# Performance work log

Measured on AMD Instinct MI355X. Metric: run time of the kernel, lower is better.

Reference implementation:

```python
import jax, jax.numpy as jnp
import numpy as np
import math

B, IN, D, H, DEPTH, E, K = 16384, 128, 512, 8, 3, 8, 2
FF, EH = 4 * D, 256          # ffn width = 4*d_model; expert hidden fixed at 256 in source
EPSILON = 0.1                # forward() default epsilon (exploration mixing)
LN_EPS = 1e-5


def _ln(x, w, b):
    m = x.mean(-1, keepdims=True)
    v = x.var(-1, keepdims=True)  # biased variance, matching nn.LayerNorm
    return (x - m) / jnp.sqrt(v + LN_EPS) * w + b


def setup_inputs() -> dict:
    key = jax.random.key(0)
    ks = jax.random.split(key, 16)
    s = 0.02
    rn = lambda k, shape: jax.random.normal(k, shape, jnp.float32) * s
    return dict(
        x=jax.random.normal(ks[0], (B, IN), jnp.float32),
        embed_w=rn(ks[1], (IN, D)), embed_b=jnp.zeros((D,), jnp.float32),
        ln1_w=jnp.ones((DEPTH, D), jnp.float32), ln1_b=jnp.zeros((DEPTH, D), jnp.float32),
        inproj_w=rn(ks[2], (DEPTH, 3 * D, D)), inproj_b=jnp.zeros((DEPTH, 3 * D), jnp.float32),
        outproj_w=rn(ks[3], (DEPTH, D, D)), outproj_b=jnp.zeros((DEPTH, D), jnp.float32),
        ln2_w=jnp.ones((DEPTH, D), jnp.float32), ln2_b=jnp.zeros((DEPTH, D), jnp.float32),
        ffn_w1=rn(ks[4], (DEPTH, D, FF)), ffn_b1=jnp.zeros((DEPTH, FF), jnp.float32),
        ffn_w2=rn(ks[5], (DEPTH, FF, D)), ffn_b2=jnp.zeros((DEPTH, D), jnp.float32),
        router_w=rn(ks[6], (D, E)), router_b=jnp.zeros((E,), jnp.float32),
        exp_w1=rn(ks[7], (E, D, EH)), exp_b1=jnp.zeros((E, EH), jnp.float32),
        exp_w2=rn(ks[8], (E, EH, D)), exp_b2=jnp.zeros((E, D), jnp.float32),
        head_ln_w=jnp.ones((D,), jnp.float32), head_ln_b=jnp.zeros((D,), jnp.float32),
        head_w=rn(ks[9], (D, 1)), head_b=jnp.zeros((1,), jnp.float32),
    )


def reference(x, embed_w, embed_b, ln1_w, ln1_b, inproj_w, inproj_b,
              outproj_w, outproj_b, ln2_w, ln2_b, ffn_w1, ffn_b1, ffn_w2, ffn_b2,
              router_w, router_b, exp_w1, exp_b1, exp_w2, exp_b2,
              head_ln_w, head_ln_b, head_w, head_b):
    h = x @ embed_w + embed_b                       # [B, D]; unsqueeze(1) -> seq_len == 1
    for l in range(DEPTH):
        g = _ln(h, ln1_w[l], ln1_b[l])
        qkv = g @ inproj_w[l].T + inproj_b[l]       # [B, 3D]
        # seq_len == 1: softmax over the single key is exactly 1, so attn(h,h,h) == out_proj(V)
        v = qkv[:, 2 * D:]
        a = v @ outproj_w[l].T + outproj_b[l]
        h = h + a
        g = _ln(h, ln2_w[l], ln2_b[l])
        h = h + jax.nn.gelu(g @ ffn_w1[l] + ffn_b1[l], approximate=False) @ ffn_w2[l] + ffn_b2[l]
    z = h                                           # squeeze(1)

    # WaggleGate
    logits = z @ router_w + router_b                # [B, E]
    probs = jax.nn.softmax(logits, axis=-1)
    probs = (1.0 - EPSILON) * probs + EPSILON / E
    wts, idx = jax.lax.top_k(probs, K)              # [B, K]
    load = probs.mean(0)
    aux = (load * jnp.log(load * E + 1e-9)).sum() / math.log(E + 1e-9)

    # dense all-expert compute + sparse top-k combine (same math as per-sample dispatch)
    hmid = jax.nn.gelu(jnp.einsum('bd,edh->ebh', z, exp_w1) + exp_b1[:, None, :], approximate=False)
    eo = jnp.einsum('ebh,ehd->ebd', hmid, exp_w2) + exp_b2[:, None, :]   # [E, B, D]
    gate = jnp.zeros((z.shape[0], E), z.dtype).at[
        jnp.arange(z.shape[0])[:, None], idx].add(wts)                    # [B, E]
    moe = jnp.einsum('be,ebd->bd', gate, eo)

    z = z + moe
    logit = (_ln(z, head_ln_w, head_ln_b) @ head_w + head_b)[:, 0]       # [B]
    return logit, aux
```

## Files before the change

kernel.cpp:

```cpp
#include <hip/hip_runtime.h>
#include <hip/hip_bf16.h>

#define B_TOK 16384
#define IN_DIM 128
#define D_DIM 512
#define DEPTH 3
#define NEXP 8
#define FF_DIM 2048
#define EH_DIM 256
#define MAXSLOT 34816
#define MAXT256 136
#define NHBLK 64

typedef __attribute__((ext_vector_type(8))) __bf16 bf16x8;
typedef __attribute__((ext_vector_type(4))) float f32x4;
typedef __attribute__((ext_vector_type(4))) unsigned short u16x4;
typedef __attribute__((ext_vector_type(8))) unsigned short u16x8;

__device__ __forceinline__ unsigned short f2bf(float f){
    unsigned int u = __float_as_uint(f);
    u += 0x7fffu + ((u >> 16) & 1u);
    return (unsigned short)(u >> 16);
}
__device__ __forceinline__ float bf2f(unsigned short u){
    return __uint_as_float(((unsigned int)u) << 16);
}
__device__ __forceinline__ float geluf(float x){
    float x2 = x * x;
    float y  = x * (0.79788456080287f + 0.03567740814183f * x2);
    y = fminf(fmaxf(y, -15.0f), 15.0f);
    float e = __expf(2.0f * y);
    float th = 1.0f - 2.0f / (e + 1.0f);
    return 0.5f * x * (1.0f + th);
}
__device__ __forceinline__ void gload_lds16(const void* g, void* l){
    __builtin_amdgcn_global_load_lds((const __attribute__((address_space(1))) unsigned int*)g,
                                     (__attribute__((address_space(3))) unsigned int*)l,
                                     16, 0, 0);
}
__device__ __forceinline__ int xcd_swizzle(int orig, int nwg){
    const int q = nwg >> 3, r = nwg & 7;
    const int xcd = orig & 7;
    const int idx = orig >> 3;
    return (xcd < r ? xcd*(q+1) : r*(q+1) + (xcd-r)*q) + idx;
}

__global__ void zero_kernel(int* a, int na, int* b, int nb){
    const int i = blockIdx.x * blockDim.x + threadIdx.x;
    if (i < na) a[i] = 0;
    if (i < nb) b[i] = 0;
}

struct ConvSeg { const float* src; unsigned short* dst; int n4; };
struct ConvArgs { ConvSeg seg[2]; };

__global__ void convert_kernel(ConvArgs a){
    const int stride = gridDim.x * blockDim.x;
    const int tid = blockIdx.x * blockDim.x + threadIdx.x;
    for (int s = 0; s < 2; ++s){
        const f32x4* src = (const f32x4*)a.seg[s].src;
        u16x4* dst = (u16x4*)a.seg[s].dst;
        const int n4 = a.seg[s].n4;
        for (int i = tid; i < n4; i += stride){
            f32x4 v = src[i];
            u16x4 o;
            o[0] = f2bf(v[0]); o[1] = f2bf(v[1]); o[2] = f2bf(v[2]); o[3] = f2bf(v[3]);
            dst[i] = o;
        }
    }
}

struct TSeg { const float* src; unsigned short* dst; int K; int N; int tileStart; };
struct TArgs { TSeg seg[26]; };

__global__ void transpose_kernel(TArgs a){
    __shared__ float t[32][33];
    const int tile = blockIdx.x;
    int s = 0;
    #pragma unroll 1
    while (s < 25 && tile >= a.seg[s+1].tileStart) ++s;
    const TSeg sg = a.seg[s];
    const int local = tile - sg.tileStart;
    const int tilesN = sg.N >> 5;
    const int k0 = (local / tilesN) << 5;
    const int n0 = (local % tilesN) << 5;
    const int tx = threadIdx.x & 31;
    const int ty = threadIdx.x >> 5;
    #pragma unroll
    for (int j = 0; j < 4; ++j)
        t[ty + j*8][tx] = sg.src[(size_t)(k0 + ty + j*8) * sg.N + n0 + tx];
    __syncthreads();
    #pragma unroll
    for (int j = 0; j < 4; ++j){
        const int n = ty + j*8;
        sg.dst[(size_t)(n0 + n) * sg.K + k0 + tx] = f2bf(t[tx][n]);
    }
}

__global__ void foldb_kernel(const float* __restrict__ outproj_w, const float* __restrict__ outproj_b,
                             const float* __restrict__ inproj_b, float* __restrict__ bfold){
    const int l = blockIdx.x, n = threadIdx.x;
    const float* Wo = outproj_w + ((size_t)l*D_DIM + n)*D_DIM;
    const float* bv = inproj_b + l*3*D_DIM + 2*D_DIM;
    float acc = outproj_b[l*D_DIM + n];
    for (int j = 0; j < D_DIM; ++j) acc += Wo[j]*bv[j];
    bfold[l*D_DIM + n] = acc;
}

__global__ void __launch_bounds__(256, 2)
gemm_bt(const unsigned short* __restrict__ A, const unsigned short* __restrict__ Bt,
        const float* __restrict__ bias, unsigned short* __restrict__ out, int NB, int N, int K)
{
    __shared__ unsigned short sh[32768];
    const int nwg = gridDim.x;
    const int wg  = xcd_swizzle(blockIdx.x, nwg);
    const int bn  = wg % NB;
    const int bm  = wg / NB;

    const int tid  = threadIdx.x;
    const int lane = tid & 63;
    const int wave = tid >> 6;
    const int wm = (wave >> 1) << 6;
    const int wn = (wave & 1) << 6;

    f32x4 acc[4][4] = {};

    const unsigned short* Abase = A + (size_t)bm * 128 * K;
    const unsigned short* Bbase = Bt + (size_t)bn * 128 * K;
    const int soff = tid * 16;

    auto STAGE = [&](int b, int kt){
        char* Ab = (char*)(sh + b*16384);
        char* Bb = (char*)(sh + b*16384 + 8192);
        #pragma unroll
        for (int s = 0; s < 4; ++s){
            const int off = s*4096 + soff;
            const int row = off >> 7, colb = off & 127;
            gload_lds16((const char*)(Abase + (size_t)row*K + kt) + colb, Ab + off);
        }
        #pragma unroll
        for (int s = 0; s < 4; ++s){
            const int off = s*4096 + soff;
            const int row = off >> 7, colb = off & 127;
            gload_lds16((const char*)(Bbase + (size_t)row*K + kt) + colb, Bb + off);
        }
    };
    auto COMPUTE = [&](int b){
        const unsigned short* Ab = sh + b*16384;
        const unsigned short* Bb = sh + b*16384 + 8192;
        #pragma unroll
        for (int ks = 0; ks < 2; ++ks){
            const int k0 = ks*32 + ((lane>>4)<<3);
            bf16x8 af[4], bfr[4];
            #pragma unroll
            for (int i=0;i<4;i++) af[i]  = *(const bf16x8*)&Ab[(wm + i*16 + (lane&15))*64 + k0];
            #pragma unroll
            for (int j=0;j<4;j++) bfr[j] = *(const bf16x8*)&Bb[(wn + j*16 + (lane&15))*64 + k0];
            #pragma unroll
            for (int i=0;i<4;i++)
                #pragma unroll
                for (int j=0;j<4;j++)
                    acc[i][j] = __builtin_amdgcn_mfma_f32_16x16x32_bf16(af[i], bfr[j], acc[i][j], 0, 0, 0);
        }
    };

    STAGE(0, 0);
    __syncthreads();
    const int nk = K >> 6;
    int cur = 0;
    for (int i = 0; i < nk; ++i){
        if (i + 1 < nk) STAGE(cur ^ 1, (i + 1) << 6);
        COMPUTE(cur);
        __syncthreads();
        cur ^= 1;
    }

    const int r0 = ((lane>>4)<<2);
    const int cc = lane & 15;
    unsigned short* Ct = sh;
    float bcol[4];
    #pragma unroll
    for (int j=0;j<4;j++) bcol[j] = bias[bn*128 + wn + j*16 + cc];
    #pragma unroll
    for (int i=0;i<4;i++)
        #pragma unroll
        for (int r=0;r<4;r++){
            const int rl = wm + i*16 + r0 + r;
            #pragma unroll
            for (int j=0;j<4;j++)
                Ct[rl*128 + wn + j*16 + cc] = f2bf(acc[i][j][r] + bcol[j]);
        }
    __syncthreads();
    const int orow = tid >> 4;
    const int ocol = (tid & 15) * 8;
    #pragma unroll
    for (int p = 0; p < 8; ++p){
        const int row = p*16 + orow;
        *(u16x8*)(&out[(size_t)(bm*128 + row)*N + bn*128 + ocol]) = *(u16x8*)&Ct[row*128 + ocol];
    }
}

__global__ void __launch_bounds__(512, 2)
gemm256sq(const unsigned short* __restrict__ A, const unsigned short* __restrict__ Bt,
          const float* __restrict__ bias, unsigned short* __restrict__ out,
          int NB, int N, int K)
{
    __shared__ __align__(16) char sh[131072];
    const int nwg = gridDim.x;
    const int wg  = xcd_swizzle(blockIdx.x, nwg);
    const int bn  = wg % NB;
    const int bm  = wg / NB;
    const int m0  = bm * 256;
    const int n0  = bn * 256;

    const int tid = threadIdx.x, lane = tid & 63, wave = tid >> 6;
    const int wr = wave >> 2;
    const int wc = wave & 3;

    const int srow = wave*16 + (lane >> 3);
    const int scol = ((lane & 7) ^ (lane >> 3)) * 8;
    const unsigned short* aptr[2][2];
    const unsigned short* bptr[2][2];
    #pragma unroll
    for (int u = 0; u < 2; ++u)
        #pragma unroll
        for (int l = 0; l < 2; ++l){
            aptr[u][l] = A  + (size_t)(m0 + u*128 + srow + l*8) * K + scol;
            bptr[u][l] = Bt + (size_t)(n0 + u*128 + srow + l*8) * K + scol;
        }
    const int sdst = wave*2048 + lane*16;

    int ch[2];
    #pragma unroll
    for (int ks = 0; ks < 2; ++ks)
        ch[ks] = ((((ks<<2) + (lane>>4)) ^ (lane & 7)) << 4);
    const int arow = wr*128 + (lane & 15);
    const int brow = wc*64  + (lane & 15);

    f32x4 acc[8][4] = {};

    auto STAGE = [&](int buf, int kt){
        #pragma unroll
        for (int u = 0; u < 2; ++u)
            #pragma unroll
            for (int l = 0; l < 2; ++l)
                gload_lds16(aptr[u][l] + kt, sh + buf*32768 + u*16384 + l*1024 + sdst);
        #pragma unroll
        for (int u = 0; u < 2; ++u)
            #pragma unroll
            for (int l = 0; l < 2; ++l)
                gload_lds16(bptr[u][l] + kt, sh + 65536 + buf*32768 + u*16384 + l*1024 + sdst);
    };
    auto COMPUTE = [&](int buf){
        bf16x8 bfr[4][2];
        #pragma unroll
        for (int nf = 0; nf < 4; ++nf)
            #pragma unroll
            for (int ks = 0; ks < 2; ++ks)
                bfr[nf][ks] = *(const bf16x8*)(sh + 65536 + buf*32768 + (brow + nf*16)*128 + ch[ks]);
        #pragma unroll
        for (int mf = 0; mf < 8; ++mf){
            bf16x8 af[2];
            #pragma unroll
            for (int ks = 0; ks < 2; ++ks)
                af[ks] = *(const bf16x8*)(sh + buf*32768 + (arow + mf*16)*128 + ch[ks]);
            #pragma unroll
            for (int nf = 0; nf < 4; ++nf)
                #pragma unroll
                for (int ks = 0; ks < 2; ++ks)
                    acc[mf][nf] = __builtin_amdgcn_mfma_f32_16x16x32_bf16(af[ks], bfr[nf][ks], acc[mf][nf], 0,0,0);
        }
    };

    STAGE(0, 0);
    __syncthreads();
    const int nk = K >> 6;
    int cur = 0;
    for (int i = 0; i < nk; ++i){
        if (i + 1 < nk) STAGE(cur ^ 1, (i + 1) << 6);
        COMPUTE(cur);
        __syncthreads();
        cur ^= 1;
    }

    unsigned short* Ct = (unsigned short*)sh;
    const int r4 = (lane >> 4) * 4;
    const int cc = lane & 15;
    #pragma unroll
    for (int nf = 0; nf < 4; ++nf){
        const int col = wc*64 + nf*16 + cc;
        const float bv = bias[n0 + col];
        #pragma unroll
        for (int mf = 0; mf < 8; ++mf)
            #pragma unroll
            for (int r = 0; r < 4; ++r){
                const int row = wr*128 + mf*16 + r4 + r;
                Ct[row*256 + col] = f2bf(geluf(acc[mf][nf][r] + bv));
            }
    }
    __syncthreads();
    #pragma unroll
    for (int p = 0; p < 16; ++p){
        const int uidx = p*512 + tid;
        const int row = uidx >> 5;
        const int cu  = uidx & 31;
        *(u16x8*)(out + (size_t)(m0 + row)*N + n0 + cu*8) = *(const u16x8*)(Ct + row*256 + cu*8);
    }
}

#define G_GELU_BF16 0
#define G_BF16_RESID 1
#define G_GATED_BF16 2

template<int EPI, int MOE, int INDIRECT>
__global__ void __launch_bounds__(512, 2)
gemm256(const unsigned short* __restrict__ A, const unsigned short* __restrict__ BtG,
        const float* __restrict__ biasG, const unsigned short* __restrict__ resid,
        const int* __restrict__ tok, const int* __restrict__ offs,
        int wstride, int bstride, const float* __restrict__ gslot,
        unsigned short* __restrict__ out, int NB, int N, int K)
{
    __shared__ __align__(16) char sh[147456];
    const int nwg = gridDim.x;
    const int wg  = xcd_swizzle(blockIdx.x, nwg);
    const int bn  = wg % NB;
    const int bm  = wg / NB;
    const int m0  = bm * 256;

    const unsigned short* Bt = BtG;
    const float* bias = biasG;
    if (MOE){
        if (m0 >= offs[8]) return;
        int e = 0;
        #pragma unroll 1
        while (offs[e+1] <= m0) ++e;
        Bt   += (size_t)e * wstride;
        bias += (size_t)e * bstride;
    }

    const int tid = threadIdx.x, lane = tid & 63, wave = tid >> 6;
    const int wm = (wave >> 1) * 64;
    const int wn = (wave & 1) * 64;

    const int srow = wave*16 + (lane >> 3);
    const int scol = ((lane & 7) ^ (lane >> 3)) * 8;
    const unsigned short* aptr[2][2];
    #pragma unroll
    for (int u = 0; u < 2; ++u)
        #pragma unroll
        for (int l = 0; l < 2; ++l){
            const int r = u*128 + srow + l*8;
            const int gr = INDIRECT ? tok[m0 + r] : (m0 + r);
            aptr[u][l] = A + (size_t)gr * K + scol;
        }
    const unsigned short* bptr[2];
    #pragma unroll
    for (int l = 0; l < 2; ++l)
        bptr[l] = Bt + (size_t)(bn*128 + srow + l*8) * K + scol;
    const int sdst = wave*2048 + lane*16;

    int aoff[2], boff[2];
    #pragma unroll
    for (int ks = 0; ks < 2; ++ks){
        const int ch = (((ks<<2) + (lane>>4)) ^ (lane & 7)) << 4;
        aoff[ks] = (wm + (lane & 15))*128 + ch;
        boff[ks] = (wn + (lane & 15))*128 + ch;
    }

    f32x4 acc[4][4] = {};

    auto STAGE = [&](int buf, int kt){
        #pragma unroll
        for (int u = 0; u < 2; ++u)
            #pragma unroll
            for (int l = 0; l < 2; ++l)
                gload_lds16(aptr[u][l] + kt, sh + buf*32768 + u*16384 + l*1024 + sdst);
        #pragma unroll
        for (int l = 0; l < 2; ++l)
            gload_lds16(bptr[l] + kt, sh + 98304 + buf*16384 + l*1024 + sdst);
    };
    auto COMPUTE = [&](int buf){
        bf16x8 bfr[4][2];
        #pragma unroll
        for (int nf = 0; nf < 4; ++nf)
            #pragma unroll
            for (int ks = 0; ks < 2; ++ks)
                bfr[nf][ks] = *(const bf16x8*)(sh + 98304 + buf*16384 + nf*2048 + boff[ks]);
        #pragma unroll
        for (int mf = 0; mf < 4; ++mf){
            bf16x8 af[2];
            #pragma unroll
            for (int ks = 0; ks < 2; ++ks)
                af[ks] = *(const bf16x8*)(sh + buf*32768 + mf*2048 + aoff[ks]);
            #pragma unroll
            for (int nf = 0; nf < 4; ++nf)
                #pragma unroll
                for (int ks = 0; ks < 2; ++ks)
                    acc[mf][nf] = __builtin_amdgcn_mfma_f32_16x16x32_bf16(af[ks], bfr[nf][ks], acc[mf][nf], 0,0,0);
        }
    };

    STAGE(0, 0);
    __syncthreads();
    const int nk = K >> 6;
    int cur = 0;
    for (int i = 0; i < nk; ++i){
        if (i + 1 < nk) STAGE(cur ^ 1, (i + 1) << 6);
        COMPUTE(cur);
        __syncthreads();
        cur ^= 1;
    }

    const int r4 = (lane >> 4) * 4;
    const int cc = lane & 15;
    if (EPI == G_BF16_RESID){
        float* ctf = (float*)sh;
        #pragma unroll
        for (int nf = 0; nf < 4; ++nf){
            const float bv = bias[bn*128 + wn + nf*16 + cc];
            #pragma unroll
            for (int mf = 0; mf < 4; ++mf)
                #pragma unroll
                for (int r = 0; r < 4; ++r){
                    const int row = wm + mf*16 + r4 + r;
                    ctf[row*128 + wn + nf*16 + cc] = acc[mf][nf][r] + bv;
                }
        }
        __syncthreads();
        #pragma unroll
        for (int p = 0; p < 8; ++p){
            const int uidx = p*512 + tid;
            const int row = uidx >> 4;
            const int cu  = uidx & 15;
            const size_t gidx = (size_t)(m0 + row)*N + bn*128 + cu*8;
            u16x8 hv = *(const u16x8*)(resid + gidx);
            u16x8 o;
            #pragma unroll
            for (int j = 0; j < 8; ++j)
                o[j] = f2bf(bf2f(hv[j]) + ctf[row*128 + cu*8 + j]);
            *(u16x8*)(out + gidx) = o;
        }
    } else {
        unsigned short* ct = (unsigned short*)sh;
        #pragma unroll
        for (int nf = 0; nf < 4; ++nf){
            const float bv = bias[bn*128 + wn + nf*16 + cc];
            #pragma unroll
            for (int mf = 0; mf < 4; ++mf)
                #pragma unroll
                for (int r = 0; r < 4; ++r){
                    const int row = wm + mf*16 + r4 + r;
                    float v = acc[mf][nf][r] + bv;
                    if (EPI == G_GELU_BF16) v = geluf(v);
                    else                    v *= gslot[m0 + row];
                    ct[row*128 + wn + nf*16 + cc] = f2bf(v);
                }
        }
        __syncthreads();
        #pragma unroll
        for (int p = 0; p < 8; ++p){
            const int uidx = p*512 + tid;
            const int row = uidx >> 4;
            const int cu  = uidx & 15;
            *(u16x8*)(out + (size_t)(m0 + row)*N + bn*128 + cu*8) =
                *(const u16x8*)(ct + row*128 + cu*8);
        }
    }
}

__global__ void ln_kernel(const unsigned short* __restrict__ x, const float* __restrict__ w,
                          const float* __restrict__ b, unsigned short* __restrict__ out)
{
    const int lane = threadIdx.x & 63;
    const int wave = threadIdx.x >> 6;
    const int row  = blockIdx.x * 4 + wave;
    u16x8 hv = *(const u16x8*)(x + (size_t)row * D_DIM + lane*8);
    float v[8];
    #pragma unroll
    for (int j = 0; j < 8; ++j) v[j] = bf2f(hv[j]);
    float s = 0.f, s2 = 0.f;
    #pragma unroll
    for (int j = 0; j < 8; ++j){ s += v[j]; s2 += v[j]*v[j]; }
    #pragma unroll
    for (int o = 32; o > 0; o >>= 1){ s += __shfl_xor(s, o); s2 += __shfl_xor(s2, o); }
    const float mean = s * (1.0f/512.0f);
    const float var  = s2 * (1.0f/512.0f) - mean*mean;
    const float inv  = 1.0f / sqrtf(var + 1e-5f);
    const int k = lane*8;
    u16x8 o;
    #pragma unroll
    for (int j = 0; j < 8; ++j) o[j] = f2bf((v[j]-mean)*inv*w[k+j] + b[k+j]);
    *(u16x8*)(out + (size_t)row*D_DIM + k) = o;
}

__global__ void router_kernel(const unsigned short* __restrict__ z, const float* __restrict__ rw,
                              const float* __restrict__ rb,
                              int2* __restrict__ idx2, float2* __restrict__ wts2,
                              float* __restrict__ bsums)
{
    __shared__ float ps[4][8];
    const int lane = threadIdx.x & 63;
    const int wave = threadIdx.x >> 6;
    const int row  = blockIdx.x * 4 + wave;
    u16x8 hv = *(const u16x8*)(z + (size_t)row * D_DIM + lane*8);
    float acc[8] = {0,0,0,0,0,0,0,0};
    #pragma unroll
    for (int j = 0; j < 8; ++j){
        const float zv = bf2f(hv[j]);
        const float* wr = rw + (size_t)(lane*8 + j) * 8;
        f32x4 w0 = *(const f32x4*)wr;
        f32x4 w1 = *(const f32x4*)(wr + 4);
        acc[0] += zv*w0[0]; acc[1] += zv*w0[1]; acc[2] += zv*w0[2]; acc[3] += zv*w0[3];
        acc[4] += zv*w1[0]; acc[5] += zv*w1[1]; acc[6] += zv*w1[2]; acc[7] += zv*w1[3];
    }
    #pragma unroll
    for (int o = 32; o > 0; o >>= 1){
        #pragma unroll
        for (int e = 0; e < 8; ++e) acc[e] += __shfl_xor(acc[e], o);
    }
    if (lane == 0){
        float p[8]; float mx = -1e30f;
        #pragma unroll
        for (int e=0;e<8;e++){ p[e] = acc[e] + rb[e]; mx = fmaxf(mx, p[e]); }
        float se = 0.f;
        #pragma unroll
        for (int e=0;e<8;e++){ p[e] = expf(p[e]-mx); se += p[e]; }
        const float sc = 0.9f / se;
        #pragma unroll
        for (int e=0;e<8;e++) p[e] = p[e]*sc + 0.0125f;
        int i1 = 0;
        #pragma unroll
        for (int e=1;e<8;e++) if (p[e] > p[i1]) i1 = e;
        int i2 = (i1 == 0) ? 1 : 0;
        for (int e=i2+1;e<8;e++) if (e != i1 && p[e] > p[i2]) i2 = e;
        idx2[row] = make_int2(i1, i2);
        wts2[row] = make_float2(p[i1], p[i2]);
        #pragma unroll
        for (int e=0;e<8;e++) ps[wave][e] = p[e];
    }
    __syncthreads();
    if (threadIdx.x < 8){
        bsums[blockIdx.x*8 + threadIdx.x] =
            ps[0][threadIdx.x] + ps[1][threadIdx.x] + ps[2][threadIdx.x] + ps[3][threadIdx.x];
    }
}

__global__ void hist_kernel(const int2* __restrict__ idx2, int* __restrict__ blockHist){
    __shared__ int hc[8];
    if (threadIdx.x < 8) hc[threadIdx.x] = 0;
    __syncthreads();
    const int t = blockIdx.x * 256 + threadIdx.x;
    const int2 ii = idx2[t];
    atomicAdd(&hc[ii.x], 1);
    atomicAdd(&hc[ii.y], 1);
    __syncthreads();
    if (threadIdx.x < 8) blockHist[blockIdx.x*8 + threadIdx.x] = hc[threadIdx.x];
}

__global__ void scan_kernel(const int* __restrict__ blockHist, int* __restrict__ offs,
                            int* __restrict__ baseArr){
    if (threadIdx.x == 0){
        int counts[8];
        #pragma unroll
        for (int e=0;e<8;e++) counts[e] = 0;
        for (int b=0;b<NHBLK;b++)
            #pragma unroll
            for (int e=0;e<8;e++) counts[e] += blockHist[b*8+e];
        int o = 0; offs[0] = 0;
        int start[8];
        #pragma unroll
        for (int e=0;e<8;e++){ start[e] = o; o += (counts[e]+255)&~255; offs[e+1] = o; }
        for (int e=0;e<8;e++){
            int cur = start[e];
            for (int b=0;b<NHBLK;b++){ baseArr[b*8+e] = cur; cur += blockHist[b*8+e]; }
        }
    }
}

__global__ void assign_kernel(const int2* __restrict__ idx2, const float2* __restrict__ wts2,
                              const int* __restrict__ baseArr, int2* __restrict__ slot_map,
                              float* __restrict__ gslot, int* __restrict__ tok)
{
    __shared__ int cur[8];
    if (threadIdx.x < 8) cur[threadIdx.x] = 0;
    __syncthreads();
    const int t = blockIdx.x * 256 + threadIdx.x;
    const int2 ii = idx2[t];
    const float2 ww = wts2[t];
    const int r1 = atomicAdd(&cur[ii.x], 1);
    const int r2 = atomicAdd(&cur[ii.y], 1);
    const int s1 = baseArr[blockIdx.x*8 + ii.x] + r1;
    const int s2 = baseArr[blockIdx.x*8 + ii.y] + r2;
    slot_map[t] = make_int2(s1, s2);
    gslot[s1] = ww.x; gslot[s2] = ww.y;
    tok[s1] = t; tok[s2] = t;
}

__global__ void aux_kernel(const float* __restrict__ bsums, float* __restrict__ out_aux)
{
    __shared__ float part[256];
    const int t = threadIdx.x;
    const int e = t & 7, chunk = t >> 3;
    float s = 0.f;
    for (int blk = chunk*128; blk < chunk*128 + 128; ++blk) s += bsums[blk*8 + e];
    part[t] = s;
    __syncthreads();
    if (t < 8){
        float tot = 0.f;
        for (int c = 0; c < 32; ++c) tot += part[c*8 + t];
        part[t] = tot;
    }
    __syncthreads();
    if (t == 0){
        float aux = 0.f;
        for (int e2 = 0; e2 < 8; ++e2){
            float load = part[e2] * (1.0f/16384.0f);
            aux += load * logf(load * 8.0f + 1e-9f);
        }
        out_aux[0] = aux / 2.0794415416798357f;
    }
}

__global__ void head_kernel(const unsigned short* __restrict__ h, const unsigned short* __restrict__ eog,
                            const int2* __restrict__ slot_map,
                            const float* __restrict__ w, const float* __restrict__ b,
                            const float* __restrict__ hw, const float* __restrict__ hb,
                            float* __restrict__ out)
{
// ... 34 lines not shown
    const float* embed_b   = (const float*)d_in[2];
    const float* ln1_w     = (const float*)d_in[3];
    const float* ln1_b     = (const float*)d_in[4];
    const float* inproj_w  = (const float*)d_in[5];
    const float* inproj_b  = (const float*)d_in[6];
    const float* outproj_w = (const float*)d_in[7];
    const float* outproj_b = (const float*)d_in[8];
    const float* ln2_w     = (const float*)d_in[9];
    const float* ln2_b     = (const float*)d_in[10];
    const float* ffn_w1    = (const float*)d_in[11];
    const float* ffn_b1    = (const float*)d_in[12];
    const float* ffn_w2    = (const float*)d_in[13];
    const float* ffn_b2    = (const float*)d_in[14];
    const float* router_w  = (const float*)d_in[15];
    const float* router_b  = (const float*)d_in[16];
    const float* exp_w1    = (const float*)d_in[17];
    const float* exp_b1    = (const float*)d_in[18];
    const float* exp_w2    = (const float*)d_in[19];
    const float* exp_b2    = (const float*)d_in[20];
    const float* head_ln_w = (const float*)d_in[21];
    const float* head_ln_b = (const float*)d_in[22];
    const float* head_w    = (const float*)d_in[23];
    const float* head_b    = (const float*)d_in[24];

    char* ws = (char*)d_ws;
    unsigned short* xbf   = (unsigned short*)(ws + 0);
    unsigned short* ebf   = (unsigned short*)(ws + 4194304);
    unsigned short* wobf  = (unsigned short*)(ws + 4325376);
    unsigned short* wvtbf = (unsigned short*)(ws + 5898240);
    unsigned short* wfold = (unsigned short*)(ws + 7471104);
    unsigned short* w1t   = (unsigned short*)(ws + 9043968);
    unsigned short* w2t   = (unsigned short*)(ws + 15335424);
    unsigned short* e1t   = (unsigned short*)(ws + 21626880);
    unsigned short* e2t   = (unsigned short*)(ws + 23724032);
    unsigned short* h     = (unsigned short*)(ws + 25821184);
    unsigned short* gbf   = (unsigned short*)(ws + 42598400);
    unsigned short* ubf   = (unsigned short*)(ws + 59375616);
    unsigned short* hmidg = ubf;
    unsigned short* eog   = (unsigned short*)(ws + 77201408);
    char* MISC = ws + 126484480;
    int*    offs     = (int*)(MISC + 0);
    float*  zbias    = (float*)(MISC + 256);
    float*  bfold    = (float*)(MISC + 2304);
    int2*   idx2     = (int2*)(MISC + 8448);
    float2* wts2     = (float2*)(MISC + 139520);
    int2*   slot_map = (int2*)(MISC + 270592);
    float*  gslot    = (float*)(MISC + 401664);
    int*    tok      = (int*)(MISC + 544768);
    float*  bsums    = (float*)(MISC + 684032);
    int*    blockHist= (int*)(MISC + 815104);
    int*    baseArr  = (int*)(MISC + 817152);
    float* out = (float*)d_out;

    zero_kernel<<<(MAXSLOT + 255)/256, 256, 0, stream>>>((int*)zbias, 512, tok, MAXSLOT);

    ConvArgs ca;
    ca.seg[0] = { x, xbf, B_TOK*IN_DIM/4 };
    ca.seg[1] = { outproj_w, wobf, DEPTH*D_DIM*D_DIM/4 };
    convert_kernel<<<1024, 256, 0, stream>>>(ca);

    TArgs ta;
    int tcur = 0, ti = 0;
    ta.seg[ti] = { embed_w, ebf, IN_DIM, D_DIM, tcur };
    tcur += (IN_DIM/32)*(D_DIM/32); ++ti;
    for (int l = 0; l < DEPTH; ++l){
        ta.seg[ti] = { ffn_w1 + (size_t)l*D_DIM*FF_DIM, w1t + (size_t)l*FF_DIM*D_DIM, D_DIM, FF_DIM, tcur };
        tcur += (D_DIM/32)*(FF_DIM/32); ++ti;
    }
    for (int l = 0; l < DEPTH; ++l){
        ta.seg[ti] = { ffn_w2 + (size_t)l*FF_DIM*D_DIM, w2t + (size_t)l*D_DIM*FF_DIM, FF_DIM, D_DIM, tcur };
        tcur += (FF_DIM/32)*(D_DIM/32); ++ti;
    }
    for (int e = 0; e < NEXP; ++e){
        ta.seg[ti] = { exp_w1 + (size_t)e*D_DIM*EH_DIM, e1t + (size_t)e*EH_DIM*D_DIM, D_DIM, EH_DIM, tcur };
        tcur += (D_DIM/32)*(EH_DIM/32); ++ti;
    }
    for (int e = 0; e < NEXP; ++e){
        ta.seg[ti] = { exp_w2 + (size_t)e*EH_DIM*D_DIM, e2t + (size_t)e*D_DIM*EH_DIM, EH_DIM, D_DIM, tcur };
        tcur += (EH_DIM/32)*(D_DIM/32); ++ti;
    }
    for (int l = 0; l < DEPTH; ++l){
        ta.seg[ti] = { inproj_w + (size_t)l*3*D_DIM*D_DIM + 2*D_DIM*D_DIM,
                       wvtbf + (size_t)l*D_DIM*D_DIM, D_DIM, D_DIM, tcur };
        tcur += (D_DIM/32)*(D_DIM/32); ++ti;
    }
    transpose_kernel<<<tcur, 256, 0, stream>>>(ta);

    foldb_kernel<<<DEPTH, D_DIM, 0, stream>>>(outproj_w, outproj_b, inproj_b, bfold);

    for (int l = 0; l < DEPTH; ++l){
        gemm_bt<<<16, 256, 0, stream>>>(
            wobf + (size_t)l*D_DIM*D_DIM, wvtbf + (size_t)l*D_DIM*D_DIM,
            zbias, wfold + (size_t)l*D_DIM*D_DIM, 4, D_DIM, D_DIM);
    }

    gemm_bt<<<(D_DIM/128)*(B_TOK/128), 256, 0, stream>>>(
        xbf, ebf, embed_b, h, D_DIM/128, D_DIM, IN_DIM);

    for (int l = 0; l < DEPTH; ++l){
        ln_kernel<<<B_TOK/4, 256, 0, stream>>>(h, ln1_w + l*D_DIM, ln1_b + l*D_DIM, gbf);
        gemm256<G_BF16_RESID,0,0><<<(B_TOK/256)*(D_DIM/128), 512, 0, stream>>>(
            gbf, wfold + (size_t)l*D_DIM*D_DIM, bfold + l*D_DIM, h,
            nullptr, nullptr, 0, 0, nullptr, h, D_DIM/128, D_DIM, D_DIM);
        ln_kernel<<<B_TOK/4, 256, 0, stream>>>(h, ln2_w + l*D_DIM, ln2_b + l*D_DIM, gbf);
        gemm256sq<<<(B_TOK/256)*(FF_DIM/256), 512, 0, stream>>>(
            gbf, w1t + (size_t)l*FF_DIM*D_DIM, ffn_b1 + l*FF_DIM, ubf, FF_DIM/256, FF_DIM, D_DIM);
        gemm256<G_BF16_RESID,0,0><<<(B_TOK/256)*(D_DIM/128), 512, 0, stream>>>(
            ubf, w2t + (size_t)l*D_DIM*FF_DIM, ffn_b2 + l*D_DIM, h,
            nullptr, nullptr, 0, 0, nullptr, h, D_DIM/128, D_DIM, FF_DIM);
    }

    router_kernel<<<B_TOK/4, 256, 0, stream>>>(h, router_w, router_b, idx2, wts2, bsums);
    aux_kernel<<<1, 256, 0, stream>>>(bsums, out + B_TOK);
    hist_kernel<<<NHBLK, 256, 0, stream>>>(idx2, blockHist);
    scan_kernel<<<1, 64, 0, stream>>>(blockHist, offs, baseArr);
    assign_kernel<<<B_TOK/256, 256, 0, stream>>>(idx2, wts2, baseArr, slot_map, gslot, tok);

    gemm256<G_GELU_BF16,1,1><<<MAXT256*(EH_DIM/128), 512, 0, stream>>>(
        h, e1t, exp_b1, nullptr, tok, offs, EH_DIM*D_DIM, EH_DIM, nullptr,
        hmidg, EH_DIM/128, EH_DIM, D_DIM);
    gemm256<G_GATED_BF16,1,0><<<MAXT256*(D_DIM/128), 512, 0, stream>>>(
        hmidg, e2t, exp_b2, nullptr, nullptr, offs, D_DIM*EH_DIM, D_DIM, gslot,
        eog, D_DIM/128, D_DIM, EH_DIM);

    head_kernel<<<B_TOK/4, 256, 0, stream>>>(h, eog, slot_map, head_ln_w, head_ln_b, head_w, head_b, out);
}
```

Measured before the change: 628.4 us.

## Software-pipeline FFN up-proj GEMM, batch fold GEMMs, parallelize foldb and scan

Rewrites the 256x256 FFN up-projection GEMM main loop into eight phases per two K-tiles. Each phase interleaves global-to-LDS loads for future tiles with MFMA work, using explicit vmcnt waits, raw s_barrier and priority raising. This aims to hide load latency better than the previous single-barrier double buffering. It also merges the three per-layer weight-fold GEMMs into one launch, makes foldb wave-parallel with a shuffle reduction, and parallelizes the routing scan across threads. The manual waitcnt scheduling is fragile and adds barriers per phase.

```diff
diff --git a/kernel.cpp b/kernel.cpp
--- a/kernel.cpp
+++ b/kernel.cpp
@@ -43,6 +43,11 @@
     const int xcd = orig & 7;
     const int idx = orig >> 3;
     return (xcd < r ? xcd*(q+1) : r*(q+1) + (xcd-r)*q) + idx;
+}
+__device__ __forceinline__ void wgbar(){
+    asm volatile("" ::: "memory");
+    __builtin_amdgcn_s_barrier();
+    asm volatile("" ::: "memory");
 }
 
 __global__ void zero_kernel(int* a, int na, int* b, int nb){
@@ -99,21 +104,32 @@
 
 __global__ void foldb_kernel(const float* __restrict__ outproj_w, const float* __restrict__ outproj_b,
                              const float* __restrict__ inproj_b, float* __restrict__ bfold){
-    const int l = blockIdx.x, n = threadIdx.x;
+    const int wave = threadIdx.x >> 6, lane = threadIdx.x & 63;
+    const int o = blockIdx.x * 4 + wave;
+    const int l = o >> 9, n = o & 511;
     const float* Wo = outproj_w + ((size_t)l*D_DIM + n)*D_DIM;
     const float* bv = inproj_b + l*3*D_DIM + 2*D_DIM;
-    float acc = outproj_b[l*D_DIM + n];
-    for (int j = 0; j < D_DIM; ++j) acc += Wo[j]*bv[j];
-    bfold[l*D_DIM + n] = acc;
+    float s = 0.f;
+    #pragma unroll
+    for (int j = 0; j < 8; ++j) s += Wo[lane + j*64] * bv[lane + j*64];
+    #pragma unroll
+    for (int off = 32; off > 0; off >>= 1) s += __shfl_xor(s, off);
+    if (lane == 0) bfold[o] = s + outproj_b[o];
 }
 
 __global__ void __launch_bounds__(256, 2)
-gemm_bt(const unsigned short* __restrict__ A, const unsigned short* __restrict__ Bt,
-        const float* __restrict__ bias, unsigned short* __restrict__ out, int NB, int N, int K)
+gemm_bt(const unsigned short* __restrict__ A0, const unsigned short* __restrict__ Bt0,
+        const float* __restrict__ bias, unsigned short* __restrict__ out0,
+        int NB, int N, int K, int nper, size_t lsa, size_t lsb, size_t lsc)
 {
     __shared__ unsigned short sh[32768];
     const int nwg = gridDim.x;
-    const int wg  = xcd_swizzle(blockIdx.x, nwg);
+    int wg  = xcd_swizzle(blockIdx.x, nwg);
+    const int layer = wg / nper;
+    wg -= layer * nper;
+    const unsigned short* A  = A0  + (size_t)layer * lsa;
+    const unsigned short* Bt = Bt0 + (size_t)layer * lsb;
+    unsigned short* out = out0 + (size_t)layer * lsc;
     const int bn  = wg % NB;
     const int bm  = wg / NB;
 
@@ -217,18 +233,26 @@
     const int wr = wave >> 2;
     const int wc = wave & 3;
 
-    const int srow = wave*16 + (lane >> 3);
-    const int scol = ((lane & 7) ^ (lane >> 3)) * 8;
-    const unsigned short* aptr[2][2];
-    const unsigned short* bptr[2][2];
-    #pragma unroll
-    for (int u = 0; u < 2; ++u)
+    const int srow8  = tid >> 3;
+    const int schunk = (tid & 7) ^ (srow8 & 7);
+    const unsigned short* Ab = A  + (size_t)m0 * K + schunk*8;
+    const unsigned short* Bb = Bt + (size_t)n0 * K + schunk*8;
+    const int ldst = (tid & 7) * 16;
+
+    auto STA = [&](int slot, int half, int kt){
         #pragma unroll
         for (int l = 0; l < 2; ++l){
-            aptr[u][l] = A  + (size_t)(m0 + u*128 + srow + l*8) * K + scol;
-            bptr[u][l] = Bt + (size_t)(n0 + u*128 + srow + l*8) * K + scol;
-        }
-    const int sdst = wave*2048 + lane*16;
+            const int r = half*128 + srow8 + l*64;
+            gload_lds16(Ab + (size_t)r*K + kt, sh + slot*32768 + r*128 + ldst);
+        }
+    };
+    auto STB = [&](int slot, int half, int kt){
+        #pragma unroll
+        for (int l = 0; l < 2; ++l){
+            const int r = half*128 + srow8 + l*64;
+            gload_lds16(Bb + (size_t)r*K + kt, sh + 65536 + slot*32768 + r*128 + ldst);
+        }
+    };
 
     int ch[2];
     #pragma unroll
@@ -238,49 +262,59 @@
     const int brow = wc*64  + (lane & 15);
 
     f32x4 acc[8][4] = {};
-
-    auto STAGE = [&](int buf, int kt){
-        #pragma unroll
-        for (int u = 0; u < 2; ++u)
-            #pragma unroll
-            for (int l = 0; l < 2; ++l)
-                gload_lds16(aptr[u][l] + kt, sh + buf*32768 + u*16384 + l*1024 + sdst);
-        #pragma unroll
-        for (int u = 0; u < 2; ++u)
-            #pragma unroll
-            for (int l = 0; l < 2; ++l)
-                gload_lds16(bptr[u][l] + kt, sh + 65536 + buf*32768 + u*16384 + l*1024 + sdst);
-    };
-    auto COMPUTE = [&](int buf){
-        bf16x8 bfr[4][2];
-        #pragma unroll
-        for (int nf = 0; nf < 4; ++nf)
-            #pragma unroll
-            for (int ks = 0; ks < 2; ++ks)
-                bfr[nf][ks] = *(const bf16x8*)(sh + 65536 + buf*32768 + (brow + nf*16)*128 + ch[ks]);
-        #pragma unroll
-        for (int mf = 0; mf < 8; ++mf){
-            bf16x8 af[2];
-            #pragma unroll
-            for (int ks = 0; ks < 2; ++ks)
-                af[ks] = *(const bf16x8*)(sh + buf*32768 + (arow + mf*16)*128 + ch[ks]);
+    bf16x8 bfr[4][2];
+
+    auto PHASE = [&](int slot, int mfb, bool rb, auto&& issue, int wait){
+        if (rb){
             #pragma unroll
             for (int nf = 0; nf < 4; ++nf)
                 #pragma unroll
                 for (int ks = 0; ks < 2; ++ks)
-                    acc[mf][nf] = __builtin_amdgcn_mfma_f32_16x16x32_bf16(af[ks], bfr[nf][ks], acc[mf][nf], 0,0,0);
-        }
+                    bfr[nf][ks] = *(const bf16x8*)(sh + 65536 + slot*32768 + (brow + nf*16)*128 + ch[ks]);
+        }
+        bf16x8 af[2][2];
+        #pragma unroll
+        for (int m2 = 0; m2 < 2; ++m2)
+            #pragma unroll
+            for (int ks = 0; ks < 2; ++ks)
+                af[m2][ks] = *(const bf16x8*)(sh + slot*32768 + (arow + (mfb+m2)*16)*128 + ch[ks]);
+        issue();
+        if (wait == 4)      asm volatile("s_waitcnt vmcnt(4)" ::: "memory");
+        else if (wait == 0) asm volatile("s_waitcnt vmcnt(0)" ::: "memory");
+        wgbar();
+        __builtin_amdgcn_s_setprio(1);
+        #pragma unroll
+        for (int m2 = 0; m2 < 2; ++m2)
+            #pragma unroll
+            for (int nf = 0; nf < 4; ++nf)
+                #pragma unroll
+                for (int ks = 0; ks < 2; ++ks)
+                    acc[mfb+m2][nf] = __builtin_amdgcn_mfma_f32_16x16x32_bf16(af[m2][ks], bfr[nf][ks], acc[mfb+m2][nf], 0,0,0);
+        __builtin_amdgcn_s_setprio(0);
+        wgbar();
     };
 
-    STAGE(0, 0);
-    __syncthreads();
+    STB(0,0,0); STB(0,1,0);
+    STA(0,0,0); STA(0,1,0);
+    STB(1,0,64); STB(1,1,64);
+    asm volatile("s_waitcnt vmcnt(4)" ::: "memory");
+    wgbar();
+
     const int nk = K >> 6;
-    int cur = 0;
-    for (int i = 0; i < nk; ++i){
-        if (i + 1 < nk) STAGE(cur ^ 1, (i + 1) << 6);
-        COMPUTE(cur);
-        __syncthreads();
-        cur ^= 1;
+    const int NT = nk >> 1;
+    for (int it = 0; it < NT; ++it){
+        const bool mp = (it + 1 < NT);
+        const int k1 = (2*it + 1) << 6;
+        const int k2 = (2*it + 2) << 6;
+        const int k3 = (2*it + 3) << 6;
+        PHASE(0, 0, true,  [&]{ STA(1,0,k1); }, -1);
+        PHASE(0, 2, false, [&]{ STA(1,1,k1); if (mp) STB(0,0,k2); }, -1);
+        PHASE(0, 4, false, [&]{ if (mp) STB(0,1,k2); }, -1);
+        PHASE(0, 6, false, [&]{}, mp ? 4 : 0);
+        PHASE(1, 0, true,  [&]{ if (mp) STA(0,0,k2); }, -1);
+        PHASE(1, 2, false, [&]{ if (mp) STA(0,1,k2); }, -1);
+        PHASE(1, 4, false, [&]{ if (mp) STB(1,0,k3); }, -1);
+        PHASE(1, 6, false, [&]{ if (mp) STB(1,1,k3); }, mp ? 4 : 0);
     }
 
     unsigned short* Ct = (unsigned short*)sh;
@@ -559,21 +593,28 @@
 
 __global__ void scan_kernel(const int* __restrict__ blockHist, int* __restrict__ offs,
                             int* __restrict__ baseArr){
-    if (threadIdx.x == 0){
-        int counts[8];
-        #pragma unroll
-        for (int e=0;e<8;e++) counts[e] = 0;
-        for (int b=0;b<NHBLK;b++)
-            #pragma unroll
-            for (int e=0;e<8;e++) counts[e] += blockHist[b*8+e];
+    __shared__ int hist[NHBLK*8];
+    __shared__ int cnt[8];
+    __shared__ int start[8];
+    const int t = threadIdx.x;
+    hist[t] = blockHist[t];
+    __syncthreads();
+    if (t < 8){
+        int c = 0;
+        #pragma unroll 1
+        for (int b = 0; b < NHBLK; ++b) c += hist[b*8 + t];
+        cnt[t] = c;
+    }
+    __syncthreads();
+    if (t == 0){
         int o = 0; offs[0] = 0;
-        int start[8];
-        #pragma unroll
-        for (int e=0;e<8;e++){ start[e] = o; o += (counts[e]+255)&~255; offs[e+1] = o; }
-        for (int e=0;e<8;e++){
-            int cur = start[e];
-            for (int b=0;b<NHBLK;b++){ baseArr[b*8+e] = cur; cur += blockHist[b*8+e]; }
-        }
+        for (int e = 0; e < 8; ++e){ start[e] = o; o += (cnt[e]+255)&~255; offs[e+1] = o; }
+    }
+    __syncthreads();
+    if (t < 8){
+        int cur = start[t];
+        #pragma unroll 1
+        for (int b = 0; b < NHBLK; ++b){ baseArr[b*8 + t] = cur; cur += hist[b*8 + t]; }
     }
 }
 
@@ -748,16 +789,15 @@
     }
     transpose_kernel<<<tcur, 256, 0, stream>>>(ta);
 
-    foldb_kernel<<<DEPTH, D_DIM, 0, stream>>>(outproj_w, outproj_b, inproj_b, bfold);
-
-    for (int l = 0; l < DEPTH; ++l){
-        gemm_bt<<<16, 256, 0, stream>>>(
-            wobf + (size_t)l*D_DIM*D_DIM, wvtbf + (size_t)l*D_DIM*D_DIM,
-            zbias, wfold + (size_t)l*D_DIM*D_DIM, 4, D_DIM, D_DIM);
-    }
+    foldb_kernel<<<DEPTH*D_DIM/4, 256, 0, stream>>>(outproj_w, outproj_b, inproj_b, bfold);
+
+    gemm_bt<<<48, 256, 0, stream>>>(
+        wobf, wvtbf, zbias, wfold, 4, D_DIM, D_DIM,
+        16, (size_t)D_DIM*D_DIM, (size_t)D_DIM*D_DIM, (size_t)D_DIM*D_DIM);
 
     gemm_bt<<<(D_DIM/128)*(B_TOK/128), 256, 0, stream>>>(
-        xbf, ebf, embed_b, h, D_DIM/128, D_DIM, IN_DIM);
+        xbf, ebf, embed_b, h, D_DIM/128, D_DIM, IN_DIM,
+        (D_DIM/128)*(B_TOK/128), 0, 0, 0);
 
     for (int l = 0; l < DEPTH; ++l){
         ln_kernel<<<B_TOK/4, 256, 0, stream>>>(h, ln1_w + l*D_DIM, ln1_b + l*D_DIM, gbf);
@@ -775,7 +815,7 @@
     router_kernel<<<B_TOK/4, 256, 0, stream>>>(h, router_w, router_b, idx2, wts2, bsums);
     aux_kernel<<<1, 256, 0, stream>>>(bsums, out + B_TOK);
     hist_kernel<<<NHBLK, 256, 0, stream>>>(idx2, blockHist);
-    scan_kernel<<<1, 64, 0, stream>>>(blockHist, offs, baseArr);
+    scan_kernel<<<1, 512, 0, stream>>>(blockHist, offs, baseArr);
     assign_kernel<<<B_TOK/256, 256, 0, stream>>>(idx2, wts2, baseArr, slot_map, gslot, tok);
 
     gemm256<G_GELU_BF16,1,1><<<MAXT256*(EH_DIM/128), 512, 0, stream>>>(
```

Result: faster. 571.0 us (-9.1%).

## Use 128x128 tile GEMM for residual layers and merge small setup kernels

Applied to the files above, without the earlier changes.

The N=512 residual GEMMs (out-projection and FFN down-projection) move from the 256-row, 512-thread gemm256 to a new 128x128, 256-thread gemm_rs kernel that adds bias and residual in its epilogue. This doubles the workgroup count for better CU coverage, at the cost of a single-buffered K loop with no load/compute overlap. Several launches are also merged: zeroing folds into the convert kernel, and the three weight-fold GEMMs become one batched launch. foldb is spread across wave-parallel reductions, and the expert scan is parallelized across threads.

```diff
diff --git a/kernel.cpp b/kernel.cpp
--- a/kernel.cpp
+++ b/kernel.cpp
@@ -45,18 +45,14 @@
     return (xcd < r ? xcd*(q+1) : r*(q+1) + (xcd-r)*q) + idx;
 }
 
-__global__ void zero_kernel(int* a, int na, int* b, int nb){
-    const int i = blockIdx.x * blockDim.x + threadIdx.x;
-    if (i < na) a[i] = 0;
-    if (i < nb) b[i] = 0;
-}
-
 struct ConvSeg { const float* src; unsigned short* dst; int n4; };
-struct ConvArgs { ConvSeg seg[2]; };
+struct ConvArgs { ConvSeg seg[2]; int* z0; int nz0; int* z1; int nz1; };
 
 __global__ void convert_kernel(ConvArgs a){
     const int stride = gridDim.x * blockDim.x;
     const int tid = blockIdx.x * blockDim.x + threadIdx.x;
+    for (int i = tid; i < a.nz0; i += stride) a.z0[i] = 0;
+    for (int i = tid; i < a.nz1; i += stride) a.z1[i] = 0;
     for (int s = 0; s < 2; ++s){
         const f32x4* src = (const f32x4*)a.seg[s].src;
         u16x4* dst = (u16x4*)a.seg[s].dst;
@@ -99,21 +95,32 @@
 
 __global__ void foldb_kernel(const float* __restrict__ outproj_w, const float* __restrict__ outproj_b,
                              const float* __restrict__ inproj_b, float* __restrict__ bfold){
-    const int l = blockIdx.x, n = threadIdx.x;
+    const int wave = threadIdx.x >> 6, lane = threadIdx.x & 63;
+    const int o = blockIdx.x * 4 + wave;
+    const int l = o >> 9, n = o & 511;
     const float* Wo = outproj_w + ((size_t)l*D_DIM + n)*D_DIM;
     const float* bv = inproj_b + l*3*D_DIM + 2*D_DIM;
-    float acc = outproj_b[l*D_DIM + n];
-    for (int j = 0; j < D_DIM; ++j) acc += Wo[j]*bv[j];
-    bfold[l*D_DIM + n] = acc;
+    float s = 0.f;
+    #pragma unroll
+    for (int j = 0; j < 8; ++j) s += Wo[lane + j*64] * bv[lane + j*64];
+    #pragma unroll
+    for (int off = 32; off > 0; off >>= 1) s += __shfl_xor(s, off);
+    if (lane == 0) bfold[o] = s + outproj_b[o];
 }
 
 __global__ void __launch_bounds__(256, 2)
-gemm_bt(const unsigned short* __restrict__ A, const unsigned short* __restrict__ Bt,
-        const float* __restrict__ bias, unsigned short* __restrict__ out, int NB, int N, int K)
+gemm_bt(const unsigned short* __restrict__ A0, const unsigned short* __restrict__ Bt0,
+        const float* __restrict__ bias, unsigned short* __restrict__ out0,
+        int NB, int N, int K, int nper, size_t lsa, size_t lsb, size_t lsc)
 {
     __shared__ unsigned short sh[32768];
     const int nwg = gridDim.x;
-    const int wg  = xcd_swizzle(blockIdx.x, nwg);
+    int wg  = xcd_swizzle(blockIdx.x, nwg);
+    const int layer = wg / nper;
+    wg -= layer * nper;
+    const unsigned short* A  = A0  + (size_t)layer * lsa;
+    const unsigned short* Bt = Bt0 + (size_t)layer * lsb;
+    unsigned short* out = out0 + (size_t)layer * lsc;
     const int bn  = wg % NB;
     const int bm  = wg / NB;
 
@@ -200,6 +207,91 @@
     }
 }
 
+__global__ void __launch_bounds__(256)
+gemm_rs(const unsigned short* __restrict__ A, const unsigned short* __restrict__ Bt,
+        const float* __restrict__ bias, const unsigned short* __restrict__ resid,
+        unsigned short* __restrict__ out, int NB, int N, int K)
+{
+    __shared__ unsigned short sh[16384];
+    const int nwg = gridDim.x;
+    const int wg  = xcd_swizzle(blockIdx.x, nwg);
+    const int bn  = wg % NB;
+    const int bm  = wg / NB;
+
+    const int tid  = threadIdx.x;
+    const int lane = tid & 63;
+    const int wave = tid >> 6;
+    const int wm = (wave >> 1) << 6;
+    const int wn = (wave & 1) << 6;
+
+    f32x4 acc[4][4] = {};
+
+    const unsigned short* Abase = A + (size_t)bm * 128 * K;
+    const unsigned short* Bbase = Bt + (size_t)bn * 128 * K;
+    const int soff = tid * 16;
+
+    const int nk = K >> 6;
+    for (int it = 0; it < nk; ++it){
+        const int kt = it << 6;
+        #pragma unroll
+        for (int s = 0; s < 4; ++s){
+            const int off = s*4096 + soff;
+            const int row = off >> 7, colb = off & 127;
+            gload_lds16((const char*)(Abase + (size_t)row*K + kt) + colb, (char*)sh + off);
+        }
+        #pragma unroll
+        for (int s = 0; s < 4; ++s){
+            const int off = s*4096 + soff;
+            const int row = off >> 7, colb = off & 127;
+            gload_lds16((const char*)(Bbase + (size_t)row*K + kt) + colb, (char*)(sh + 8192) + off);
+        }
+        __syncthreads();
+        #pragma unroll
+        for (int ks = 0; ks < 2; ++ks){
+            const int k0 = ks*32 + ((lane>>4)<<3);
+            bf16x8 af[4], bfr[4];
+            #pragma unroll
+            for (int i=0;i<4;i++) af[i]  = *(const bf16x8*)&sh[(wm + i*16 + (lane&15))*64 + k0];
+            #pragma unroll
+            for (int j=0;j<4;j++) bfr[j] = *(const bf16x8*)&sh[8192 + (wn + j*16 + (lane&15))*64 + k0];
+            #pragma unroll
+            for (int i=0;i<4;i++)
+                #pragma unroll
+                for (int j=0;j<4;j++)
+                    acc[i][j] = __builtin_amdgcn_mfma_f32_16x16x32_bf16(af[i], bfr[j], acc[i][j], 0, 0, 0);
+        }
+        __syncthreads();
+    }
+
+    const int r0 = ((lane>>4)<<2);
+    const int cc = lane & 15;
+    unsigned short* Ct = sh;
+    float bcol[4];
+    #pragma unroll
+    for (int j=0;j<4;j++) bcol[j] = bias[bn*128 + wn + j*16 + cc];
+    #pragma unroll
+    for (int i=0;i<4;i++)
+        #pragma unroll
+        for (int r=0;r<4;r++){
+            const int rl = wm + i*16 + r0 + r;
+            const size_t grow = (size_t)(bm*128 + rl) * N + bn*128;
+            #pragma unroll
+            for (int j=0;j<4;j++){
+                const int col = wn + j*16 + cc;
+                const float v = acc[i][j][r] + bcol[j] + bf2f(resid[grow + col]);
+                Ct[rl*128 + col] = f2bf(v);
+            }
+        }
+    __syncthreads();
+    const int orow = tid >> 4;
+    const int ocol = (tid & 15) * 8;
+    #pragma unroll
+    for (int p = 0; p < 8; ++p){
+        const int row = p*16 + orow;
+        *(u16x8*)(&out[(size_t)(bm*128 + row)*N + bn*128 + ocol]) = *(u16x8*)&Ct[row*128 + ocol];
+    }
+}
+
 __global__ void __launch_bounds__(512, 2)
 gemm256sq(const unsigned short* __restrict__ A, const unsigned short* __restrict__ Bt,
           const float* __restrict__ bias, unsigned short* __restrict__ out,
@@ -309,13 +401,12 @@
 }
 
 #define G_GELU_BF16 0
-#define G_BF16_RESID 1
 #define G_GATED_BF16 2
 
-template<int EPI, int MOE, int INDIRECT>
+template<int EPI, int INDIRECT>
 __global__ void __launch_bounds__(512, 2)
 gemm256(const unsigned short* __restrict__ A, const unsigned short* __restrict__ BtG,
-        const float* __restrict__ biasG, const unsigned short* __restrict__ resid,
+        const float* __restrict__ biasG,
         const int* __restrict__ tok, const int* __restrict__ offs,
         int wstride, int bstride, const float* __restrict__ gslot,
         unsigned short* __restrict__ out, int NB, int N, int K)
@@ -327,16 +418,12 @@
     const int bm  = wg / NB;
     const int m0  = bm * 256;
 
-    const unsigned short* Bt = BtG;
-    const float* bias = biasG;
-    if (MOE){
-        if (m0 >= offs[8]) return;
-        int e = 0;
-        #pragma unroll 1
-        while (offs[e+1] <= m0) ++e;
-        Bt   += (size_t)e * wstride;
-        bias += (size_t)e * bstride;
-    }
+    if (m0 >= offs[8]) return;
+    int e = 0;
+    #pragma unroll 1
+    while (offs[e+1] <= m0) ++e;
+    const unsigned short* Bt = BtG + (size_t)e * wstride;
+    const float* bias = biasG + (size_t)e * bstride;
 
     const int tid = threadIdx.x, lane = tid & 63, wave = tid >> 6;
     const int wm = (wave >> 1) * 64;
@@ -413,58 +500,29 @@
 
     const int r4 = (lane >> 4) * 4;
     const int cc = lane & 15;
-    if (EPI == G_BF16_RESID){
-        float* ctf = (float*)sh;
-        #pragma unroll
-        for (int nf = 0; nf < 4; ++nf){
-            const float bv = bias[bn*128 + wn + nf*16 + cc];
-            #pragma unroll
-            for (int mf = 0; mf < 4; ++mf)
-                #pragma unroll
-                for (int r = 0; r < 4; ++r){
-                    const int row = wm + mf*16 + r4 + r;
-                    ctf[row*128 + wn + nf*16 + cc] = acc[mf][nf][r] + bv;
-                }
-        }
-        __syncthreads();
-        #pragma unroll
-        for (int p = 0; p < 8; ++p){
-            const int uidx = p*512 + tid;
-            const int row = uidx >> 4;
-            const int cu  = uidx & 15;
-            const size_t gidx = (size_t)(m0 + row)*N + bn*128 + cu*8;
-            u16x8 hv = *(const u16x8*)(resid + gidx);
-            u16x8 o;
-            #pragma unroll
-            for (int j = 0; j < 8; ++j)
-                o[j] = f2bf(bf2f(hv[j]) + ctf[row*128 + cu*8 + j]);
-            *(u16x8*)(out + gidx) = o;
-        }
-    } else {
-        unsigned short* ct = (unsigned short*)sh;
-        #pragma unroll
-        for (int nf = 0; nf < 4; ++nf){
-            const float bv = bias[bn*128 + wn + nf*16 + cc];
-            #pragma unroll
-            for (int mf = 0; mf < 4; ++mf)
-                #pragma unroll
-                for (int r = 0; r < 4; ++r){
-                    const int row = wm + mf*16 + r4 + r;
-                    float v = acc[mf][nf][r] + bv;
-                    if (EPI == G_GELU_BF16) v = geluf(v);
-                    else                    v *= gslot[m0 + row];
-                    ct[row*128 + wn + nf*16 + cc] = f2bf(v);
-                }
-        }
-        __syncthreads();
-        #pragma unroll
-        for (int p = 0; p < 8; ++p){
-            const int uidx = p*512 + tid;
-            const int row = uidx >> 4;
-            const int cu  = uidx & 15;
-            *(u16x8*)(out + (size_t)(m0 + row)*N + bn*128 + cu*8) =
-                *(const u16x8*)(ct + row*128 + cu*8);
-        }
+    unsigned short* ct = (unsigned short*)sh;
+    #pragma unroll
+    for (int nf = 0; nf < 4; ++nf){
+        const float bv = bias[bn*128 + wn + nf*16 + cc];
+        #pragma unroll
+        for (int mf = 0; mf < 4; ++mf)
+            #pragma unroll
+            for (int r = 0; r < 4; ++r){
+                const int row = wm + mf*16 + r4 + r;
+                float v = acc[mf][nf][r] + bv;
+                if (EPI == G_GELU_BF16) v = geluf(v);
+                else                    v *= gslot[m0 + row];
+                ct[row*128 + wn + nf*16 + cc] = f2bf(v);
+            }
+    }
+    __syncthreads();
+    #pragma unroll
+    for (int p = 0; p < 8; ++p){
+        const int uidx = p*512 + tid;
+        const int row = uidx >> 4;
+        const int cu  = uidx & 15;
+        *(u16x8*)(out + (size_t)(m0 + row)*N + bn*128 + cu*8) =
+            *(const u16x8*)(ct + row*128 + cu*8);
     }
 }
 
@@ -559,21 +617,28 @@
 
 __global__ void scan_kernel(const int* __restrict__ blockHist, int* __restrict__ offs,
                             int* __restrict__ baseArr){
-    if (threadIdx.x == 0){
-        int counts[8];
-        #pragma unroll
-        for (int e=0;e<8;e++) counts[e] = 0;
-        for (int b=0;b<NHBLK;b++)
-            #pragma unroll
-            for (int e=0;e<8;e++) counts[e] += blockHist[b*8+e];
+    __shared__ int hist[NHBLK*8];
+    __shared__ int cnt[8];
+    __shared__ int start[8];
+    const int t = threadIdx.x;
+    hist[t] = blockHist[t];
+    __syncthreads();
+    if (t < 8){
+        int c = 0;
+        #pragma unroll 1
+        for (int b = 0; b < NHBLK; ++b) c += hist[b*8 + t];
+        cnt[t] = c;
+    }
+    __syncthreads();
+    if (t == 0){
         int o = 0; offs[0] = 0;
-        int start[8];
-        #pragma unroll
-        for (int e=0;e<8;e++){ start[e] = o; o += (counts[e]+255)&~255; offs[e+1] = o; }
-        for (int e=0;e<8;e++){
-            int cur = start[e];
-            for (int b=0;b<NHBLK;b++){ baseArr[b*8+e] = cur; cur += blockHist[b*8+e]; }
-        }
+        for (int e = 0; e < 8; ++e){ start[e] = o; o += (cnt[e]+255)&~255; offs[e+1] = o; }
+    }
+    __syncthreads();
+    if (t < 8){
+        int cur = start[t];
+        #pragma unroll 1
+        for (int b = 0; b < NHBLK; ++b){ baseArr[b*8 + t] = cur; cur += hist[b*8 + t]; }
     }
 }
 
@@ -714,11 +779,11 @@
     int*    baseArr  = (int*)(MISC + 817152);
     float* out = (float*)d_out;
 
-    zero_kernel<<<(MAXSLOT + 255)/256, 256, 0, stream>>>((int*)zbias, 512, tok, MAXSLOT);
-
     ConvArgs ca;
     ca.seg[0] = { x, xbf, B_TOK*IN_DIM/4 };
     ca.seg[1] = { outproj_w, wobf, DEPTH*D_DIM*D_DIM/4 };
+    ca.z0 = (int*)zbias; ca.nz0 = 512;
+    ca.z1 = tok;         ca.nz1 = MAXSLOT;
     convert_kernel<<<1024, 256, 0, stream>>>(ca);
 
     TArgs ta;
@@ -748,41 +813,38 @@
     }
     transpose_kernel<<<tcur, 256, 0, stream>>>(ta);
 
-    foldb_kernel<<<DEPTH, D_DIM, 0, stream>>>(outproj_w, outproj_b, inproj_b, bfold);
-
-    for (int l = 0; l < DEPTH; ++l){
-        gemm_bt<<<16, 256, 0, stream>>>(
-            wobf + (size_t)l*D_DIM*D_DIM, wvtbf + (size_t)l*D_DIM*D_DIM,
-            zbias, wfold + (size_t)l*D_DIM*D_DIM, 4, D_DIM, D_DIM);
-    }
+    foldb_kernel<<<DEPTH*D_DIM/4, 256, 0, stream>>>(outproj_w, outproj_b, inproj_b, bfold);
+
+    gemm_bt<<<48, 256, 0, stream>>>(
+        wobf, wvtbf, zbias, wfold, 4, D_DIM, D_DIM,
+        16, (size_t)D_DIM*D_DIM, (size_t)D_DIM*D_DIM, (size_t)D_DIM*D_DIM);
 
     gemm_bt<<<(D_DIM/128)*(B_TOK/128), 256, 0, stream>>>(
-        xbf, ebf, embed_b, h, D_DIM/128, D_DIM, IN_DIM);
+        xbf, ebf, embed_b, h, D_DIM/128, D_DIM, IN_DIM,
+        (D_DIM/128)*(B_TOK/128), 0, 0, 0);
 
     for (int l = 0; l < DEPTH; ++l){
         ln_kernel<<<B_TOK/4, 256, 0, stream>>>(h, ln1_w + l*D_DIM, ln1_b + l*D_DIM, gbf);
-        gemm256<G_BF16_RESID,0,0><<<(B_TOK/256)*(D_DIM/128), 512, 0, stream>>>(
-            gbf, wfold + (size_t)l*D_DIM*D_DIM, bfold + l*D_DIM, h,
-            nullptr, nullptr, 0, 0, nullptr, h, D_DIM/128, D_DIM, D_DIM);
+        gemm_rs<<<(D_DIM/128)*(B_TOK/128), 256, 0, stream>>>(
+            gbf, wfold + (size_t)l*D_DIM*D_DIM, bfold + l*D_DIM, h, h, D_DIM/128, D_DIM, D_DIM);
         ln_kernel<<<B_TOK/4, 256, 0, stream>>>(h, ln2_w + l*D_DIM, ln2_b + l*D_DIM, gbf);
         gemm256sq<<<(B_TOK/256)*(FF_DIM/256), 512, 0, stream>>>(
             gbf, w1t + (size_t)l*FF_DIM*D_DIM, ffn_b1 + l*FF_DIM, ubf, FF_DIM/256, FF_DIM, D_DIM);
-        gemm256<G_BF16_RESID,0,0><<<(B_TOK/256)*(D_DIM/128), 512, 0, stream>>>(
-            ubf, w2t + (size_t)l*D_DIM*FF_DIM, ffn_b2 + l*D_DIM, h,
-            nullptr, nullptr, 0, 0, nullptr, h, D_DIM/128, D_DIM, FF_DIM);
+        gemm_rs<<<(D_DIM/128)*(B_TOK/128), 256, 0, stream>>>(
+            ubf, w2t + (size_t)l*D_DIM*FF_DIM, ffn_b2 + l*D_DIM, h, h, D_DIM/128, D_DIM, FF_DIM);
     }
 
     router_kernel<<<B_TOK/4, 256, 0, stream>>>(h, router_w, router_b, idx2, wts2, bsums);
     aux_kernel<<<1, 256, 0, stream>>>(bsums, out + B_TOK);
     hist_kernel<<<NHBLK, 256, 0, stream>>>(idx2, blockHist);
-    scan_kernel<<<1, 64, 0, stream>>>(blockHist, offs, baseArr);
+    scan_kernel<<<1, 512, 0, stream>>>(blockHist, offs, baseArr);
     assign_kernel<<<B_TOK/256, 256, 0, stream>>>(idx2, wts2, baseArr, slot_map, gslot, tok);
 
-    gemm256<G_GELU_BF16,1,1><<<MAXT256*(EH_DIM/128), 512, 0, stream>>>(
-        h, e1t, exp_b1, nullptr, tok, offs, EH_DIM*D_DIM, EH_DIM, nullptr,
+    gemm256<G_GELU_BF16,1><<<MAXT256*(EH_DIM/128), 512, 0, stream>>>(
+        h, e1t, exp_b1, tok, offs, EH_DIM*D_DIM, EH_DIM, nullptr,
         hmidg, EH_DIM/128, EH_DIM, D_DIM);
-    gemm256<G_GATED_BF16,1,0><<<MAXT256*(D_DIM/128), 512, 0, stream>>>(
-        hmidg, e2t, exp_b2, nullptr, nullptr, offs, D_DIM*EH_DIM, D_DIM, gslot,
+    gemm256<G_GATED_BF16,0><<<MAXT256*(D_DIM/128), 512, 0, stream>>>(
+        hmidg, e2t, exp_b2, nullptr, offs, D_DIM*EH_DIM, D_DIM, gslot,
         eog, D_DIM/128, D_DIM, EH_DIM);
 
     head_kernel<<<B_TOK/4, 256, 0, stream>>>(h, eog, slot_map, head_ln_w, head_ln_b, head_w, head_b, out);
```

Measured after the change: 636.3 us. No clear change (+1.3%).
